# Kernel tuning notes

Hardware: AMD Instinct MI355X
Metric: run time of the kernel (lower is better)

## Reference

```python
import jax, jax.numpy as jnp
import numpy as np

MODES = (16, 16)

def setup_inputs() -> dict:
    key = jax.random.key(0)
    ks = jax.random.split(key, 8)
    B, Cin, Cout, H, W = 16, 64, 64, 128, 128
    scale = 1.0 / (Cin * Cout)
    return {
        "x": jax.random.normal(ks[0], (B, Cin, H, W), jnp.float32),
        "t_emb": jax.random.normal(ks[1], (B, 512), jnp.float32),
        "weight_real": jax.random.normal(ks[2], (Cin, Cout, *MODES), jnp.float32) * 2 * scale - scale,
        "weight_imag": jax.random.normal(ks[3], (Cin, Cout, *MODES), jnp.float32) * 2 * scale - scale,
        "bypass_w": jax.random.normal(ks[4], (Cout, Cin), jnp.float32) * 0.05,
        "bypass_b": jax.random.normal(ks[5], (Cout,), jnp.float32) * 0.05,
        "temb_w": jax.random.normal(ks[6], (Cin, 512), jnp.float32) * 0.02,
        "temb_b": jax.random.normal(ks[7], (Cin,), jnp.float32) * 0.02,
    }

def reference(x, t_emb, weight_real, weight_imag, bypass_w, bypass_b, temb_w, temb_b):
    mk, ml = MODES
    H, W = x.shape[-2:]
    xf = x.astype(jnp.float32)
    # truncated spectral conv: rfft2 (ortho), keep low-mode corner only
    x_fft = jnp.fft.rfftn(xf, axes=(-2, -1), norm="ortho")[:, :, :mk, :ml]
    weight = weight_real + 1j * weight_imag  # [i, o, k, l]
    out_fft = jnp.einsum("bikl,iokl->bokl", x_fft, weight)
    x_spec = jnp.fft.irfftn(out_fft, s=(H, W), axes=(-2, -1), norm="ortho")
    # 1x1 conv bypass
    byp = jnp.einsum("bihw,oi->bohw", xf, bypass_w) + bypass_b[None, :, None, None]
    out = jax.nn.gelu(x_spec + byp, approximate=False)
    # temb fusion: x + Linear(silu(temb))[:, :, None, None]
    silu_t = t_emb * jax.nn.sigmoid(t_emb)
    proj = silu_t @ temb_w.T + temb_b  # [B, C]
    out = out + proj[:, :, None, None]
    return out
```

## Files before the change

### kernel.cpp

```cpp
#include <hip/hip_runtime.h>
#include <cmath>

#define TWO_PI_128 0.04908738521234052f

typedef __attribute__((ext_vector_type(8))) short bf16x8;
typedef __attribute__((ext_vector_type(4))) float f32x4;

__device__ inline unsigned short f2bf(float v) {
  unsigned u = __float_as_uint(v);
  unsigned r = (u + 0x7FFFu + ((u >> 16) & 1u)) >> 16;
  return (unsigned short)r;
}

__global__ __launch_bounds__(256) void front_kernel(
    const float* __restrict__ x, float* __restrict__ xfr_t,
    float* __restrict__ xfi_t, const float* __restrict__ wr,
    const float* __restrict__ wi, float* __restrict__ wt_r,
    float* __restrict__ wt_i, const float* __restrict__ t_emb,
    const float* __restrict__ temb_w, const float* __restrict__ temb_b,
    float* __restrict__ proj, float2* __restrict__ Tck,
    unsigned short* __restrict__ Tspec) {
  __shared__ union SM {
    struct {
      unsigned short x1[32 * 136];
      float red[8 * 256];
    } f;
    float tile[32][33];
    struct {
      float silu[512];
      float part[64][4];
    } p;
  } sm;

  const int bid = blockIdx.x;
  const int t = threadIdx.x;

  if (bid >= 3088) {
    if (t < 128) {
      float dS, dC;
      sincosf(TWO_PI_128 * (float)t, &dS, &dC);
      float ck = 1.f, sk = 0.f;
      for (int k = 0; k < 16; ++k) {
        Tck[t * 16 + k] = make_float2(ck, sk);
        float tt = sk * dS, uu = ck * dS;
        ck = fmaf(ck, dC, -tt);
        sk = fmaf(sk, dC, uu);
      }
    } else {
      const int wn = t - 128;
      float st, ct;
      sincosf(TWO_PI_128 * (float)wn, &st, &ct);
#pragma unroll
      for (int half = 0; half < 2; ++half) {
        float ss, cc;
        sincosf(TWO_PI_128 * (float)(wn * (half * 8)), &ss, &cc);
        for (int j = 0; j < 8; ++j) {
          Tspec[wn * 32 + half * 8 + j] = f2bf(cc);
          Tspec[wn * 32 + 16 + half * 8 + j] = f2bf(-ss);
          float nc = cc * ct - ss * st;
          ss = ss * ct + cc * st;
          cc = nc;
        }
      }
    }
    return;
  }

  if (bid >= 3072) {
    const int b = bid - 3072;
    for (int j = t; j < 512; j += 256) {
      float v = t_emb[b * 512 + j];
      sm.p.silu[j] = v / (1.f + __expf(-v));
    }
    __syncthreads();
    const int o = t >> 2, part = t & 3;
    const float* wrow = temb_w + o * 512 + part * 128;
    const float* srow = sm.p.silu + part * 128;
    float acc = 0.f;
#pragma unroll 8
    for (int j = 0; j < 128; ++j) acc = fmaf(srow[j], wrow[j], acc);
    sm.p.part[o][part] = acc;
    __syncthreads();
    if (part == 0) {
      proj[b * 64 + o] = sm.p.part[o][0] + sm.p.part[o][1] + sm.p.part[o][2] +
                         sm.p.part[o][3] + temb_b[o];
    }
    return;
  }

  if (bid >= 1024) {
    const int flat = bid - 1024;
    const int tensor = flat >> 10;
    const int rem = flat & 1023;
    const int io0 = (rem >> 3) * 32, kl0 = (rem & 7) * 32;
    const float* src = tensor ? wi : wr;
    float* dst = tensor ? wt_i : wt_r;
    const int ty = t >> 3, tx = t & 7;
    float4 v = *(const float4*)(src + (size_t)(io0 + ty) * 256 + kl0 + 4 * tx);
    sm.tile[ty][4 * tx + 0] = v.x;
    sm.tile[ty][4 * tx + 1] = v.y;
    sm.tile[ty][4 * tx + 2] = v.z;
    sm.tile[ty][4 * tx + 3] = v.w;
    __syncthreads();
    float4 o;
    o.x = sm.tile[4 * tx + 0][ty];
    o.y = sm.tile[4 * tx + 1][ty];
    o.z = sm.tile[4 * tx + 2][ty];
    o.w = sm.tile[4 * tx + 3][ty];
    *(float4*)(dst + (size_t)(kl0 + ty) * 4096 + io0 + 4 * tx) = o;
    return;
  }

  const int plane = bid;
  const int wv = t >> 6, lane = t & 63, l15 = lane & 15, quad = lane >> 4;

  union U8 {
    bf16x8 v;
    unsigned short u[8];
  };

  float dC, dS;
  sincosf(TWO_PI_128 * (float)l15, &dS, &dC);

  U8 a_re[4], a_im[4];
#pragma unroll
  for (int ks = 0; ks < 4; ++ks) {
    const int w0 = ks * 32 + quad * 8;
    float c, s;
    sincosf(TWO_PI_128 * (float)((l15 * w0) & 127), &s, &c);
#pragma unroll
    for (int j = 0; j < 8; ++j) {
      a_re[ks].u[j] = f2bf(c);
      a_im[ks].u[j] = f2bf(-s);
      float nc = c * dC - s * dS;
      s = s * dC + c * dS;
      c = nc;
    }
  }

  const float* xp = x + (size_t)plane * 16384;
  f32x4 acc[2][2];
#pragma unroll
  for (int mt = 0; mt < 2; ++mt)
#pragma unroll
    for (int nt = 0; nt < 2; ++nt) acc[mt][nt] = (f32x4){0.f, 0.f, 0.f, 0.f};

#pragma unroll
  for (int ks = 0; ks < 4; ++ks) {
#pragma unroll
    for (int nt = 0; nt < 2; ++nt) {
      const float* src =
          xp + (size_t)((wv * 2 + nt) * 16 + l15) * 128 + ks * 32 + quad * 8;
      float4 v0 = *(const float4*)src;
      float4 v1 = *(const float4*)(src + 4);
      U8 bx;
      bx.u[0] = f2bf(v0.x);
      bx.u[1] = f2bf(v0.y);
      bx.u[2] = f2bf(v0.z);
      bx.u[3] = f2bf(v0.w);
      bx.u[4] = f2bf(v1.x);
      bx.u[5] = f2bf(v1.y);
      bx.u[6] = f2bf(v1.z);
      bx.u[7] = f2bf(v1.w);
      acc[0][nt] = __builtin_amdgcn_mfma_f32_16x16x32_bf16(a_re[ks].v, bx.v,
                                                           acc[0][nt], 0, 0, 0);
      acc[1][nt] = __builtin_amdgcn_mfma_f32_16x16x32_bf16(a_im[ks].v, bx.v,
                                                           acc[1][nt], 0, 0, 0);
    }
  }

#pragma unroll
  for (int mt = 0; mt < 2; ++mt)
#pragma unroll
    for (int nt = 0; nt < 2; ++nt)
#pragma unroll
      for (int r = 0; r < 4; ++r)
        sm.f.x1[(mt * 16 + quad * 4 + r) * 136 + (wv * 2 + nt) * 16 + l15] =
            f2bf(acc[mt][nt][r]);
  __syncthreads();

  f32x4 accre = (f32x4){0.f, 0.f, 0.f, 0.f};
  f32x4 accim = (f32x4){0.f, 0.f, 0.f, 0.f};
#pragma unroll
  for (int kl2 = 0; kl2 < 2; ++kl2) {
    const int ks2 = wv * 2 + kl2;
    const int hb = (ks2 & 3) * 32 + quad * 8;
    const int imh = ks2 >> 2;
    float c, s;
    sincosf(TWO_PI_128 * (float)((l15 * hb) & 127), &s, &c);
    U8 ar, ai;
#pragma unroll
    for (int j = 0; j < 8; ++j) {
      if (!imh) {
        ar.u[j] = f2bf(c);
        ai.u[j] = f2bf(-s);
      } else {
        ar.u[j] = f2bf(s);
        ai.u[j] = f2bf(c);
      }
      float nc = c * dC - s * dS;
      s = s * dC + c * dS;
      c = nc;
    }
    bf16x8 bfrag = *(const bf16x8*)(sm.f.x1 + (imh * 16 + l15) * 136 + hb);
    accre =
        __builtin_amdgcn_mfma_f32_16x16x32_bf16(ar.v, bfrag, accre, 0, 0, 0);
    accim =
        __builtin_amdgcn_mfma_f32_16x16x32_bf16(ai.v, bfrag, accim, 0, 0, 0);
  }
  *(f32x4*)(sm.f.red + (wv * 2) * 256 + lane * 4) = accre;
  *(f32x4*)(sm.f.red + (wv * 2 + 1) * 256 + lane * 4) = accim;
  __syncthreads();

  const float re =
      sm.f.red[t] + sm.f.red[512 + t] + sm.f.red[1024 + t] + sm.f.red[1536 + t];
  const float im = sm.f.red[256 + t] + sm.f.red[768 + t] + sm.f.red[1280 + t] +
                   sm.f.red[1792 + t];
  const int k = (t >> 6) * 4 + (t & 3), l = (t >> 2) & 15;
  xfr_t[(size_t)(k * 16 + l) * 1024 + plane] = re * 0.0078125f;
  xfi_t[(size_t)(k * 16 + l) * 1024 + plane] = im * 0.0078125f;
}

__global__ __launch_bounds__(1024) void modemix_kernel(
    const float* __restrict__ xfr_t, const float* __restrict__ xfi_t,
    const float* __restrict__ wt_r, const float* __restrict__ wt_i,
    float* __restrict__ ofr, float* __restrict__ ofi) {
  __shared__ float s_xr[1024], s_xi[1024];
  __shared__ float s_wr[4096], s_wi[4096];
  const int kl = blockIdx.x;
  const int t = threadIdx.x;
  if (t < 256)
    ((float4*)s_xr)[t] = ((const float4*)(xfr_t + (size_t)kl * 1024))[t];
  else if (t < 512)
    ((float4*)s_xi)[t - 256] =
        ((const float4*)(xfi_t + (size_t)kl * 1024))[t - 256];
  ((float4*)s_wr)[t] = ((const float4*)(wt_r + (size_t)kl * 4096))[t];
  ((float4*)s_wi)[t] = ((const float4*)(wt_i + (size_t)kl * 4096))[t];
  __syncthreads();
  const int b = t >> 6;
  const int o = t & 63;
  const float* xrp = s_xr + b * 64;
  const float* xip = s_xi + b * 64;
  float ar0 = 0.f, ar1 = 0.f, ai0 = 0.f, ai1 = 0.f;
#pragma unroll 4
  for (int i = 0; i < 64; ++i) {
    float wrv = s_wr[i * 64 + o], wiv = s_wi[i * 64 + o];
    float xr = xrp[i], xi = xip[i];
    ar0 = fmaf(xr, wrv, ar0);
    ar1 = fmaf(xi, wiv, ar1);
    ai0 = fmaf(xr, wiv, ai0);
    ai1 = fmaf(xi, wrv, ai1);
  }
  ofr[(size_t)(b * 64 + o) * 256 + kl] = ar0 - ar1;
  ofi[(size_t)(b * 64 + o) * 256 + kl] = ai0 + ai1;
}

__global__ __launch_bounds__(256, 4) void final_kernel(
    const float* __restrict__ x, const float* __restrict__ bw,
    const float* __restrict__ bb, const float* __restrict__ proj,
    const float* __restrict__ ofr, const float* __restrict__ ofi,
    const float2* __restrict__ Tck, const unsigned short* __restrict__ Tspec,
    float* __restrict__ out) {
#define AR 104
  __shared__ unsigned short s_A[64 * AR];
  __shared__ float s_bb[64];
  __shared__ float s_pb[64];
  const int h = blockIdx.x, b = blockIdx.y, t = threadIdx.x;
  const int wv = t >> 6, lane = t & 63;
  const int l15 = lane & 15, quad = lane >> 4;
  const int n0w = wv * 32;

  float xv[32];
  {
    const float* xbase = x + (size_t)b * 1048576 + (size_t)h * 128;
#pragma unroll
    for (int ks2 = 0; ks2 < 2; ++ks2)
#pragma unroll
      for (int nt = 0; nt < 2; ++nt)
#pragma unroll
        for (int j = 0; j < 8; ++j)
          xv[(ks2 * 2 + nt) * 8 + j] =
              xbase[(size_t)(ks2 * 32 + quad * 8 + j) * 16384 + n0w + nt * 16 +
                    l15];
  }

  bf16x8 tsf[2];
#pragma unroll
  for (int nt = 0; nt < 2; ++nt)
    tsf[nt] = *(const bf16x8*)(Tspec + (n0w + nt * 16 + l15) * 32 + quad * 8);

  if (t < 64)
    s_bb[t] = bb[t];
  else if (t < 128)
    s_pb[t - 64] = proj[b * 64 + (t - 64)];

  {
    const int o = t >> 2, q = t & 3;
    const float4* src = (const float4*)(bw + o * 64 + q * 16);
    unsigned int u[8];
#pragma unroll
    for (int m = 0; m < 4; ++m) {
      float4 v = src[m];
      u[2 * m] = (unsigned)f2bf(v.x) | ((unsigned)f2bf(v.y) << 16);
      u[2 * m + 1] = (unsigned)f2bf(v.z) | ((unsigned)f2bf(v.w) << 16);
    }
    uint4* dst = (uint4*)(s_A + o * AR + q * 16);
    dst[0] = make_uint4(u[0], u[1], u[2], u[3]);
    dst[1] = make_uint4(u[4], u[5], u[6], u[7]);
  }
  {
    const int o = t >> 2, lq = t & 3;
    const float* FR = ofr + (size_t)(b * 64 + o) * 256 + lq * 4;
    const float* FI = ofi + (size_t)(b * 64 + o) * 256 + lq * 4;
    const float2* tckrow = Tck + h * 16;
    float yr[4] = {0.f, 0.f, 0.f, 0.f};
    float yi[4] = {0.f, 0.f, 0.f, 0.f};
#pragma unroll 4
    for (int k = 0; k < 16; ++k) {
      float4 fr = *(const float4*)(FR + k * 16);
      float4 fi = *(const float4*)(FI + k * 16);
      const float2 cs = tckrow[k];
      const float ck = cs.x, sk = cs.y;
      yr[0] = fmaf(fr.x, ck, yr[0]);
      yr[0] = fmaf(-fi.x, sk, yr[0]);
      yi[0] = fmaf(fi.x, ck, yi[0]);
      yi[0] = fmaf(fr.x, sk, yi[0]);
      yr[1] = fmaf(fr.y, ck, yr[1]);
      yr[1] = fmaf(-fi.y, sk, yr[1]);
      yi[1] = fmaf(fi.y, ck, yi[1]);
      yi[1] = fmaf(fr.y, sk, yi[1]);
      yr[2] = fmaf(fr.z, ck, yr[2]);
      yr[2] = fmaf(-fi.z, sk, yr[2]);
      yi[2] = fmaf(fi.z, ck, yi[2]);
      yi[2] = fmaf(fr.z, sk, yi[2]);
      yr[3] = fmaf(fr.w, ck, yr[3]);
      yr[3] = fmaf(-fi.w, sk, yr[3]);
      yi[3] = fmaf(fi.w, ck, yi[3]);
      yi[3] = fmaf(fr.w, sk, yi[3]);
    }
    const float scl0 = (lq == 0) ? 0.0078125f : 0.015625f;
    unsigned ur0 = (unsigned)f2bf(yr[0] * scl0) |
                   ((unsigned)f2bf(yr[1] * 0.015625f) << 16);
    unsigned ur1 = (unsigned)f2bf(yr[2] * 0.015625f) |
                   ((unsigned)f2bf(yr[3] * 0.015625f) << 16);
    unsigned ui0 = (unsigned)f2bf(yi[0] * scl0) |
                   ((unsigned)f2bf(yi[1] * 0.015625f) << 16);
    unsigned ui1 = (unsigned)f2bf(yi[2] * 0.015625f) |
                   ((unsigned)f2bf(yi[3] * 0.015625f) << 16);
    *(uint2*)(s_A + o * AR + 64 + lq * 4) = make_uint2(ur0, ur1);
    *(uint2*)(s_A + o * AR + 64 + 16 + lq * 4) = make_uint2(ui0, ui1);
  }
  __syncthreads();

  f32x4 acc[4][2];
#pragma unroll
  for (int mt = 0; mt < 4; ++mt) {
    f32x4 bv = *(const f32x4*)(s_bb + mt * 16 + quad * 4);
    acc[mt][0] = bv;
    acc[mt][1] = bv;
  }

#pragma unroll
  for (int ks2 = 0; ks2 < 2; ++ks2) {
    union {
      bf16x8 v;
      unsigned short u[8];
    } bx[2];
#pragma unroll
    for (int nt = 0; nt < 2; ++nt)
#pragma unroll
      for (int j = 0; j < 8; ++j)
        bx[nt].u[j] = f2bf(xv[(ks2 * 2 + nt) * 8 + j]);
#pragma unroll
    for (int mt = 0; mt < 4; ++mt) {
      bf16x8 a =
          *(const bf16x8*)(s_A + (mt * 16 + l15) * AR + ks2 * 32 + quad * 8);
      acc[mt][0] = __builtin_amdgcn_mfma_f32_16x16x32_bf16(a, bx[0].v,
                                                           acc[mt][0], 0, 0, 0);
      acc[mt][1] = __builtin_amdgcn_mfma_f32_16x16x32_bf16(a, bx[1].v,
                                                           acc[mt][1], 0, 0, 0);
    }
  }

#pragma unroll
  for (int mt = 0; mt < 4; ++mt) {
    bf16x8 a = *(const bf16x8*)(s_A + (mt * 16 + l15) * AR + 64 + quad * 8);
    acc[mt][0] =
        __builtin_amdgcn_mfma_f32_16x16x32_bf16(a, tsf[0], acc[mt][0], 0, 0, 0);
    acc[mt][1] =
        __builtin_amdgcn_mfma_f32_16x16x32_bf16(a, tsf[1], acc[mt][1], 0, 0, 0);
  }

#pragma unroll
  for (int mt = 0; mt < 4; ++mt) {
    f32x4 pv = *(const f32x4*)(s_pb + mt * 16 + quad * 4);
#pragma unroll
    for (int nt = 0; nt < 2; ++nt) {
      const int wcol = n0w + nt * 16 + l15;
#pragma unroll
      for (int r = 0; r < 4; ++r) {
        const int o = mt * 16 + quad * 4 + r;
        float v = acc[mt][nt][r];
        float g = fmaf(0.5f * v, 1.f + erff(v * 0.70710678f), pv[r]);
        out[((size_t)(b * 64 + o) * 128 + h) * 128 + wcol] = g;
      }
    }
  }
#undef AR
}

extern "C" void kernel_launch(void* const* d_in, const int* in_sizes, int n_in,
                              void* d_out, int out_size, void* d_ws,
                              size_t ws_size, hipStream_t stream) {
  (void)in_sizes;
  (void)n_in;
  (void)out_size;
  (void)ws_size;
  const float* x = (const float*)d_in[0];
  const float* t_emb = (const float*)d_in[1];
  const float* wr = (const float*)d_in[2];
  const float* wi = (const float*)d_in[3];
  const float* bw = (const float*)d_in[4];
  const float* bb = (const float*)d_in[5];
  const float* tw = (const float*)d_in[6];
  const float* tb = (const float*)d_in[7];
  float* out = (float*)d_out;

  char* ws = (char*)d_ws;
  float* proj = (float*)(ws);
  float* ofr = (float*)(ws + ((size_t)1 << 20));
  float* ofi = (float*)(ws + ((size_t)2 << 20));
  float* xfr_t = (float*)(ws + ((size_t)3 << 20));
  float* xfi_t = (float*)(ws + ((size_t)4 << 20));
  float* wt_r = (float*)(ws + ((size_t)5 << 20));
  float* wt_i = (float*)(ws + ((size_t)9 << 20));
  float2* Tck = (float2*)(ws + ((size_t)13 << 20));
  unsigned short* Tspec = (unsigned short*)(ws + ((size_t)13 << 20) + 65536);

  front_kernel<<<3089, 256, 0, stream>>>(x, xfr_t, xfi_t, wr, wi, wt_r, wt_i,
                                         t_emb, tw, tb, proj, Tck, Tspec);
  modemix_kernel<<<256, 1024, 0, stream>>>(xfr_t, xfi_t, wt_r, wt_i, ofr, ofi);
  final_kernel<<<dim3(128, 16), 256, 0, stream>>>(x, bw, bb, proj, ofr, ofi,
                                                  Tck, Tspec, out);
}
```

Before: 168.4 us.

## Write bf16 copy of x in front kernel and read it in final kernel

The front kernel already converts x to bf16 for its DFT MFMA, and now also stores that bf16 copy in a transposed [b][h][c][w] layout in workspace. The final kernel reads the bf16 copy instead of re-reading fp32 x with strided loads and converting again, which halves the bytes it reads for x and drops the conversion. The cost is an extra 32 MB write in the front kernel. The final kernel also loses its min-blocks launch-bounds hint, so register allocation may change.

```diff
diff --git a/kernel.cpp b/kernel.cpp
--- a/kernel.cpp
+++ b/kernel.cpp
@@ -19,7 +19,7 @@
     float* __restrict__ wt_i, const float* __restrict__ t_emb,
     const float* __restrict__ temb_w, const float* __restrict__ temb_b,
     float* __restrict__ proj, float2* __restrict__ Tck,
-    unsigned short* __restrict__ Tspec) {
+    unsigned short* __restrict__ Tspec, unsigned short* __restrict__ xbf) {
   __shared__ union SM {
     struct {
       unsigned short x1[32 * 136];
@@ -112,6 +112,7 @@
   }
 
   const int plane = bid;
+  const int xb_ = plane >> 6, xi_ = plane & 63;
   const int wv = t >> 6, lane = t & 63, l15 = lane & 15, quad = lane >> 4;
 
   union U8 {
@@ -149,8 +150,8 @@
   for (int ks = 0; ks < 4; ++ks) {
 #pragma unroll
     for (int nt = 0; nt < 2; ++nt) {
-      const float* src =
-          xp + (size_t)((wv * 2 + nt) * 16 + l15) * 128 + ks * 32 + quad * 8;
+      const int row = (wv * 2 + nt) * 16 + l15;
+      const float* src = xp + (size_t)row * 128 + ks * 32 + quad * 8;
       float4 v0 = *(const float4*)src;
       float4 v1 = *(const float4*)(src + 4);
       U8 bx;
@@ -162,6 +163,8 @@
       bx.u[5] = f2bf(v1.y);
       bx.u[6] = f2bf(v1.z);
       bx.u[7] = f2bf(v1.w);
+      *(uint4*)(xbf + ((size_t)(xb_ * 128 + row) * 64 + xi_) * 128 + ks * 32 +
+                quad * 8) = *(const uint4*)&bx;
       acc[0][nt] = __builtin_amdgcn_mfma_f32_16x16x32_bf16(a_re[ks].v, bx.v,
                                                            acc[0][nt], 0, 0, 0);
       acc[1][nt] = __builtin_amdgcn_mfma_f32_16x16x32_bf16(a_im[ks].v, bx.v,
@@ -255,8 +258,8 @@
   ofi[(size_t)(b * 64 + o) * 256 + kl] = ai0 + ai1;
 }
 
-__global__ __launch_bounds__(256, 4) void final_kernel(
-    const float* __restrict__ x, const float* __restrict__ bw,
+__global__ __launch_bounds__(256) void final_kernel(
+    const unsigned short* __restrict__ xbf, const float* __restrict__ bw,
     const float* __restrict__ bb, const float* __restrict__ proj,
     const float* __restrict__ ofr, const float* __restrict__ ofi,
     const float2* __restrict__ Tck, const unsigned short* __restrict__ Tspec,
@@ -270,18 +273,22 @@
   const int l15 = lane & 15, quad = lane >> 4;
   const int n0w = wv * 32;
 
-  float xv[32];
+  union FB {
+    bf16x8 v;
+    unsigned short u[8];
+  };
+  FB bx[4];
   {
-    const float* xbase = x + (size_t)b * 1048576 + (size_t)h * 128;
+    const unsigned short* xb =
+        xbf + (size_t)(b * 128 + h) * 8192 + n0w + l15;
 #pragma unroll
     for (int ks2 = 0; ks2 < 2; ++ks2)
 #pragma unroll
-      for (int nt = 0; nt < 2; ++nt)
-#pragma unroll
-        for (int j = 0; j < 8; ++j)
-          xv[(ks2 * 2 + nt) * 8 + j] =
-              xbase[(size_t)(ks2 * 32 + quad * 8 + j) * 16384 + n0w + nt * 16 +
-                    l15];
+      for (int nt = 0; nt < 2; ++nt) {
+        const unsigned short* s = xb + (ks2 * 32 + quad * 8) * 128 + nt * 16;
+#pragma unroll
+        for (int j = 0; j < 8; ++j) bx[ks2 * 2 + nt].u[j] = s[j * 128];
+      }
   }
 
   bf16x8 tsf[2];
@@ -362,23 +369,14 @@
 
 #pragma unroll
   for (int ks2 = 0; ks2 < 2; ++ks2) {
-    union {
-      bf16x8 v;
-      unsigned short u[8];
-    } bx[2];
-#pragma unroll
-    for (int nt = 0; nt < 2; ++nt)
-#pragma unroll
-      for (int j = 0; j < 8; ++j)
-        bx[nt].u[j] = f2bf(xv[(ks2 * 2 + nt) * 8 + j]);
 #pragma unroll
     for (int mt = 0; mt < 4; ++mt) {
       bf16x8 a =
           *(const bf16x8*)(s_A + (mt * 16 + l15) * AR + ks2 * 32 + quad * 8);
-      acc[mt][0] = __builtin_amdgcn_mfma_f32_16x16x32_bf16(a, bx[0].v,
-                                                           acc[mt][0], 0, 0, 0);
-      acc[mt][1] = __builtin_amdgcn_mfma_f32_16x16x32_bf16(a, bx[1].v,
-                                                           acc[mt][1], 0, 0, 0);
+      acc[mt][0] = __builtin_amdgcn_mfma_f32_16x16x32_bf16(
+          a, bx[ks2 * 2 + 0].v, acc[mt][0], 0, 0, 0);
+      acc[mt][1] = __builtin_amdgcn_mfma_f32_16x16x32_bf16(
+          a, bx[ks2 * 2 + 1].v, acc[mt][1], 0, 0, 0);
     }
   }
 
@@ -436,10 +434,11 @@
   float* wt_i = (float*)(ws + ((size_t)9 << 20));
   float2* Tck = (float2*)(ws + ((size_t)13 << 20));
   unsigned short* Tspec = (unsigned short*)(ws + ((size_t)13 << 20) + 65536);
+  unsigned short* xbf = (unsigned short*)(ws + ((size_t)16 << 20));
 
   front_kernel<<<3089, 256, 0, stream>>>(x, xfr_t, xfi_t, wr, wi, wt_r, wt_i,
-                                         t_emb, tw, tb, proj, Tck, Tspec);
+                                         t_emb, tw, tb, proj, Tck, Tspec, xbf);
   modemix_kernel<<<256, 1024, 0, stream>>>(xfr_t, xfi_t, wt_r, wt_i, ofr, ofi);
-  final_kernel<<<dim3(128, 16), 256, 0, stream>>>(x, bw, bb, proj, ofr, ofi,
+  final_kernel<<<dim3(128, 16), 256, 0, stream>>>(xbf, bw, bb, proj, ofr, ofi,
                                                   Tck, Tspec, out);
 }
```

Result: slower. 173.8 us (+3.2%).

## Process two rows per final block and hoist front-kernel x loads

Applied to the files above, without the earlier changes.

The final kernel now handles two h rows per block, with half as many blocks. The bypass-weight conversion and the spectral inverse-FFT stage along k are shared across both rows, computing two Tck rows at once into a wider shared tile. The front kernel issues all of its x loads up front, before the twiddle sincos setup, so memory latency overlaps with that setup. The trade-off is fewer blocks and more registers per thread, with the min-occupancy launch bound dropped, so occupancy may fall.

```diff
diff --git a/kernel.cpp b/kernel.cpp
--- a/kernel.cpp
+++ b/kernel.cpp
@@ -119,6 +119,20 @@
     unsigned short u[8];
   };
 
+  float4 xv[16];
+  {
+    const float* xp = x + (size_t)plane * 16384;
+#pragma unroll
+    for (int ks = 0; ks < 4; ++ks)
+#pragma unroll
+      for (int nt = 0; nt < 2; ++nt) {
+        const float* src =
+            xp + (size_t)((wv * 2 + nt) * 16 + l15) * 128 + ks * 32 + quad * 8;
+        xv[(ks * 2 + nt) * 2 + 0] = *(const float4*)src;
+        xv[(ks * 2 + nt) * 2 + 1] = *(const float4*)(src + 4);
+      }
+  }
+
   float dC, dS;
   sincosf(TWO_PI_128 * (float)l15, &dS, &dC);
 
@@ -138,7 +152,6 @@
     }
   }
 
-  const float* xp = x + (size_t)plane * 16384;
   f32x4 acc[2][2];
 #pragma unroll
   for (int mt = 0; mt < 2; ++mt)
@@ -149,10 +162,8 @@
   for (int ks = 0; ks < 4; ++ks) {
 #pragma unroll
     for (int nt = 0; nt < 2; ++nt) {
-      const float* src =
-          xp + (size_t)((wv * 2 + nt) * 16 + l15) * 128 + ks * 32 + quad * 8;
-      float4 v0 = *(const float4*)src;
-      float4 v1 = *(const float4*)(src + 4);
+      const float4 v0 = xv[(ks * 2 + nt) * 2 + 0];
+      const float4 v1 = xv[(ks * 2 + nt) * 2 + 1];
       U8 bx;
       bx.u[0] = f2bf(v0.x);
       bx.u[1] = f2bf(v0.y);
@@ -255,34 +266,20 @@
   ofi[(size_t)(b * 64 + o) * 256 + kl] = ai0 + ai1;
 }
 
-__global__ __launch_bounds__(256, 4) void final_kernel(
+__global__ __launch_bounds__(256) void final_kernel(
     const float* __restrict__ x, const float* __restrict__ bw,
     const float* __restrict__ bb, const float* __restrict__ proj,
     const float* __restrict__ ofr, const float* __restrict__ ofi,
     const float2* __restrict__ Tck, const unsigned short* __restrict__ Tspec,
     float* __restrict__ out) {
-#define AR 104
+#define AR 136
   __shared__ unsigned short s_A[64 * AR];
   __shared__ float s_bb[64];
   __shared__ float s_pb[64];
-  const int h = blockIdx.x, b = blockIdx.y, t = threadIdx.x;
+  const int hp = blockIdx.x, b = blockIdx.y, t = threadIdx.x;
   const int wv = t >> 6, lane = t & 63;
   const int l15 = lane & 15, quad = lane >> 4;
   const int n0w = wv * 32;
-
-  float xv[32];
-  {
-    const float* xbase = x + (size_t)b * 1048576 + (size_t)h * 128;
-#pragma unroll
-    for (int ks2 = 0; ks2 < 2; ++ks2)
-#pragma unroll
-      for (int nt = 0; nt < 2; ++nt)
-#pragma unroll
-        for (int j = 0; j < 8; ++j)
-          xv[(ks2 * 2 + nt) * 8 + j] =
-              xbase[(size_t)(ks2 * 32 + quad * 8 + j) * 16384 + n0w + nt * 16 +
-                    l15];
-  }
 
   bf16x8 tsf[2];
 #pragma unroll
@@ -312,97 +309,115 @@
     const int o = t >> 2, lq = t & 3;
     const float* FR = ofr + (size_t)(b * 64 + o) * 256 + lq * 4;
     const float* FI = ofi + (size_t)(b * 64 + o) * 256 + lq * 4;
-    const float2* tckrow = Tck + h * 16;
-    float yr[4] = {0.f, 0.f, 0.f, 0.f};
-    float yi[4] = {0.f, 0.f, 0.f, 0.f};
+    const float2* tck0 = Tck + (hp * 2) * 16;
+    const float2* tck1 = Tck + (hp * 2 + 1) * 16;
+    float yr0[4] = {0.f, 0.f, 0.f, 0.f}, yi0[4] = {0.f, 0.f, 0.f, 0.f};
+    float yr1[4] = {0.f, 0.f, 0.f, 0.f}, yi1[4] = {0.f, 0.f, 0.f, 0.f};
 #pragma unroll 4
     for (int k = 0; k < 16; ++k) {
       float4 fr = *(const float4*)(FR + k * 16);
       float4 fi = *(const float4*)(FI + k * 16);
-      const float2 cs = tckrow[k];
-      const float ck = cs.x, sk = cs.y;
-      yr[0] = fmaf(fr.x, ck, yr[0]);
-      yr[0] = fmaf(-fi.x, sk, yr[0]);
-      yi[0] = fmaf(fi.x, ck, yi[0]);
-      yi[0] = fmaf(fr.x, sk, yi[0]);
-      yr[1] = fmaf(fr.y, ck, yr[1]);
-      yr[1] = fmaf(-fi.y, sk, yr[1]);
-      yi[1] = fmaf(fi.y, ck, yi[1]);
-      yi[1] = fmaf(fr.y, sk, yi[1]);
-      yr[2] = fmaf(fr.z, ck, yr[2]);
-      yr[2] = fmaf(-fi.z, sk, yr[2]);
-      yi[2] = fmaf(fi.z, ck, yi[2]);
-      yi[2] = fmaf(fr.z, sk, yi[2]);
-      yr[3] = fmaf(fr.w, ck, yr[3]);
-      yr[3] = fmaf(-fi.w, sk, yr[3]);
-      yi[3] = fmaf(fi.w, ck, yi[3]);
-      yi[3] = fmaf(fr.w, sk, yi[3]);
+      const float2 c0 = tck0[k], c1 = tck1[k];
+      const float frv[4] = {fr.x, fr.y, fr.z, fr.w};
+      const float fiv[4] = {fi.x, fi.y, fi.z, fi.w};
+#pragma unroll
+      for (int c = 0; c < 4; ++c) {
+        yr0[c] = fmaf(frv[c], c0.x, yr0[c]);
+        yr0[c] = fmaf(-fiv[c], c0.y, yr0[c]);
+        yi0[c] = fmaf(fiv[c], c0.x, yi0[c]);
+        yi0[c] = fmaf(frv[c], c0.y, yi0[c]);
+        yr1[c] = fmaf(frv[c], c1.x, yr1[c]);
+        yr1[c] = fmaf(-fiv[c], c1.y, yr1[c]);
+        yi1[c] = fmaf(fiv[c], c1.x, yi1[c]);
+        yi1[c] = fmaf(frv[c], c1.y, yi1[c]);
+      }
     }
     const float scl0 = (lq == 0) ? 0.0078125f : 0.015625f;
-    unsigned ur0 = (unsigned)f2bf(yr[0] * scl0) |
-                   ((unsigned)f2bf(yr[1] * 0.015625f) << 16);
-    unsigned ur1 = (unsigned)f2bf(yr[2] * 0.015625f) |
-                   ((unsigned)f2bf(yr[3] * 0.015625f) << 16);
-    unsigned ui0 = (unsigned)f2bf(yi[0] * scl0) |
-                   ((unsigned)f2bf(yi[1] * 0.015625f) << 16);
-    unsigned ui1 = (unsigned)f2bf(yi[2] * 0.015625f) |
-                   ((unsigned)f2bf(yi[3] * 0.015625f) << 16);
+    unsigned ur0 = (unsigned)f2bf(yr0[0] * scl0) |
+                   ((unsigned)f2bf(yr0[1] * 0.015625f) << 16);
+    unsigned ur1 = (unsigned)f2bf(yr0[2] * 0.015625f) |
+                   ((unsigned)f2bf(yr0[3] * 0.015625f) << 16);
+    unsigned ui0 = (unsigned)f2bf(yi0[0] * scl0) |
+                   ((unsigned)f2bf(yi0[1] * 0.015625f) << 16);
+    unsigned ui1 = (unsigned)f2bf(yi0[2] * 0.015625f) |
+                   ((unsigned)f2bf(yi0[3] * 0.015625f) << 16);
     *(uint2*)(s_A + o * AR + 64 + lq * 4) = make_uint2(ur0, ur1);
-    *(uint2*)(s_A + o * AR + 64 + 16 + lq * 4) = make_uint2(ui0, ui1);
+    *(uint2*)(s_A + o * AR + 80 + lq * 4) = make_uint2(ui0, ui1);
+    unsigned vr0 = (unsigned)f2bf(yr1[0] * scl0) |
+                   ((unsigned)f2bf(yr1[1] * 0.015625f) << 16);
+    unsigned vr1 = (unsigned)f2bf(yr1[2] * 0.015625f) |
+                   ((unsigned)f2bf(yr1[3] * 0.015625f) << 16);
+    unsigned vi0 = (unsigned)f2bf(yi1[0] * scl0) |
+                   ((unsigned)f2bf(yi1[1] * 0.015625f) << 16);
+    unsigned vi1 = (unsigned)f2bf(yi1[2] * 0.015625f) |
+                   ((unsigned)f2bf(yi1[3] * 0.015625f) << 16);
+    *(uint2*)(s_A + o * AR + 96 + lq * 4) = make_uint2(vr0, vr1);
+    *(uint2*)(s_A + o * AR + 112 + lq * 4) = make_uint2(vi0, vi1);
   }
   __syncthreads();
 
-  f32x4 acc[4][2];
-#pragma unroll
-  for (int mt = 0; mt < 4; ++mt) {
-    f32x4 bv = *(const f32x4*)(s_bb + mt * 16 + quad * 4);
-    acc[mt][0] = bv;
-    acc[mt][1] = bv;
-  }
-
-#pragma unroll
-  for (int ks2 = 0; ks2 < 2; ++ks2) {
-    union {
-      bf16x8 v;
-      unsigned short u[8];
-    } bx[2];
-#pragma unroll
-    for (int nt = 0; nt < 2; ++nt)
-#pragma unroll
-      for (int j = 0; j < 8; ++j)
-        bx[nt].u[j] = f2bf(xv[(ks2 * 2 + nt) * 8 + j]);
+#pragma unroll
+  for (int hh = 0; hh < 2; ++hh) {
+    const int h = hp * 2 + hh;
+
+    f32x4 acc[4][2];
 #pragma unroll
     for (int mt = 0; mt < 4; ++mt) {
-      bf16x8 a =
-          *(const bf16x8*)(s_A + (mt * 16 + l15) * AR + ks2 * 32 + quad * 8);
-      acc[mt][0] = __builtin_amdgcn_mfma_f32_16x16x32_bf16(a, bx[0].v,
+      f32x4 bv = *(const f32x4*)(s_bb + mt * 16 + quad * 4);
+      acc[mt][0] = bv;
+      acc[mt][1] = bv;
+    }
+
+    const float* xrow = x + (size_t)b * 1048576 + (size_t)h * 128 + n0w + l15;
+#pragma unroll
+    for (int ks = 0; ks < 64; ks += 32) {
+      union {
+        bf16x8 v;
+        unsigned short u[8];
+      } bx[2];
+#pragma unroll
+      for (int nt = 0; nt < 2; ++nt) {
+        float xv[8];
+#pragma unroll
+        for (int j = 0; j < 8; ++j)
+          xv[j] = xrow[(size_t)(ks + quad * 8 + j) * 16384 + nt * 16];
+#pragma unroll
+        for (int j = 0; j < 8; ++j) bx[nt].u[j] = f2bf(xv[j]);
+      }
+#pragma unroll
+      for (int mt = 0; mt < 4; ++mt) {
+        bf16x8 a =
+            *(const bf16x8*)(s_A + (mt * 16 + l15) * AR + ks + quad * 8);
+        acc[mt][0] = __builtin_amdgcn_mfma_f32_16x16x32_bf16(
+            a, bx[0].v, acc[mt][0], 0, 0, 0);
+        acc[mt][1] = __builtin_amdgcn_mfma_f32_16x16x32_bf16(
+            a, bx[1].v, acc[mt][1], 0, 0, 0);
+      }
+    }
+
+#pragma unroll
+    for (int mt = 0; mt < 4; ++mt) {
+      bf16x8 a = *(const bf16x8*)(s_A + (mt * 16 + l15) * AR + 64 + hh * 32 +
+                                  quad * 8);
+      acc[mt][0] = __builtin_amdgcn_mfma_f32_16x16x32_bf16(a, tsf[0],
                                                            acc[mt][0], 0, 0, 0);
-      acc[mt][1] = __builtin_amdgcn_mfma_f32_16x16x32_bf16(a, bx[1].v,
+      acc[mt][1] = __builtin_amdgcn_mfma_f32_16x16x32_bf16(a, tsf[1],
                                                            acc[mt][1], 0, 0, 0);
     }
-  }
-
-#pragma unroll
-  for (int mt = 0; mt < 4; ++mt) {
-    bf16x8 a = *(const bf16x8*)(s_A + (mt * 16 + l15) * AR + 64 + quad * 8);
-    acc[mt][0] =
-        __builtin_amdgcn_mfma_f32_16x16x32_bf16(a, tsf[0], acc[mt][0], 0, 0, 0);
-    acc[mt][1] =
-        __builtin_amdgcn_mfma_f32_16x16x32_bf16(a, tsf[1], acc[mt][1], 0, 0, 0);
-  }
-
-#pragma unroll
-  for (int mt = 0; mt < 4; ++mt) {
-    f32x4 pv = *(const f32x4*)(s_pb + mt * 16 + quad * 4);
-#pragma unroll
-    for (int nt = 0; nt < 2; ++nt) {
-      const int wcol = n0w + nt * 16 + l15;
-#pragma unroll
-      for (int r = 0; r < 4; ++r) {
-        const int o = mt * 16 + quad * 4 + r;
-        float v = acc[mt][nt][r];
-        float g = fmaf(0.5f * v, 1.f + erff(v * 0.70710678f), pv[r]);
-        out[((size_t)(b * 64 + o) * 128 + h) * 128 + wcol] = g;
+
+#pragma unroll
+    for (int mt = 0; mt < 4; ++mt) {
+      f32x4 pv = *(const f32x4*)(s_pb + mt * 16 + quad * 4);
+#pragma unroll
+      for (int nt = 0; nt < 2; ++nt) {
+        const int wcol = n0w + nt * 16 + l15;
+#pragma unroll
+        for (int r = 0; r < 4; ++r) {
+          const int o = mt * 16 + quad * 4 + r;
+          float v = acc[mt][nt][r];
+          float g = fmaf(0.5f * v, 1.f + erff(v * 0.70710678f), pv[r]);
+          out[((size_t)(b * 64 + o) * 128 + h) * 128 + wcol] = g;
+        }
       }
     }
   }
@@ -440,6 +455,6 @@
   front_kernel<<<3089, 256, 0, stream>>>(x, xfr_t, xfi_t, wr, wi, wt_r, wt_i,
                                          t_emb, tw, tb, proj, Tck, Tspec);
   modemix_kernel<<<256, 1024, 0, stream>>>(xfr_t, xfi_t, wt_r, wt_i, ofr, ofi);
-  final_kernel<<<dim3(128, 16), 256, 0, stream>>>(x, bw, bb, proj, ofr, ofi,
-                                                  Tck, Tspec, out);
+  final_kernel<<<dim3(64, 16), 256, 0, stream>>>(x, bw, bb, proj, ofr, ofi,
+                                                 Tck, Tspec, out);
 }
```

Measured after the change: 171.2 us. No clear change (+1.7%).

## Split final kernel over output-channel halves to double grid parallelism

Applied to the files above, without the earlier changes.

The final kernel now launches a third grid dimension of 2, so each block computes 32 of the 64 output channels. This shrinks per-block shared memory, accumulators and the inverse-DFT work per thread. The x tile is loaded inside the MFMA loop instead of being prefetched into 32 registers, and the occupancy hint in the launch bounds is dropped. The cost is that every x row is now read by two blocks, doubling x traffic for the bypass GEMM.

```diff
diff --git a/kernel.cpp b/kernel.cpp
--- a/kernel.cpp
+++ b/kernel.cpp
@@ -255,34 +255,21 @@
   ofi[(size_t)(b * 64 + o) * 256 + kl] = ai0 + ai1;
 }
 
-__global__ __launch_bounds__(256, 4) void final_kernel(
+__global__ __launch_bounds__(256) void final_kernel(
     const float* __restrict__ x, const float* __restrict__ bw,
     const float* __restrict__ bb, const float* __restrict__ proj,
     const float* __restrict__ ofr, const float* __restrict__ ofi,
     const float2* __restrict__ Tck, const unsigned short* __restrict__ Tspec,
     float* __restrict__ out) {
 #define AR 104
-  __shared__ unsigned short s_A[64 * AR];
+  __shared__ unsigned short s_A[32 * AR];
   __shared__ float s_bb[64];
   __shared__ float s_pb[64];
   const int h = blockIdx.x, b = blockIdx.y, t = threadIdx.x;
+  const int ob = blockIdx.z * 32;
   const int wv = t >> 6, lane = t & 63;
   const int l15 = lane & 15, quad = lane >> 4;
   const int n0w = wv * 32;
-
-  float xv[32];
-  {
-    const float* xbase = x + (size_t)b * 1048576 + (size_t)h * 128;
-#pragma unroll
-    for (int ks2 = 0; ks2 < 2; ++ks2)
-#pragma unroll
-      for (int nt = 0; nt < 2; ++nt)
-#pragma unroll
-        for (int j = 0; j < 8; ++j)
-          xv[(ks2 * 2 + nt) * 8 + j] =
-              xbase[(size_t)(ks2 * 32 + quad * 8 + j) * 16384 + n0w + nt * 16 +
-                    l15];
-  }
 
   bf16x8 tsf[2];
 #pragma unroll
@@ -294,9 +281,9 @@
   else if (t < 128)
     s_pb[t - 64] = proj[b * 64 + (t - 64)];
 
-  {
+  if (t < 128) {
     const int o = t >> 2, q = t & 3;
-    const float4* src = (const float4*)(bw + o * 64 + q * 16);
+    const float4* src = (const float4*)(bw + (ob + o) * 64 + q * 16);
     unsigned int u[8];
 #pragma unroll
     for (int m = 0; m < 4; ++m) {
@@ -309,72 +296,63 @@
     dst[1] = make_uint4(u[4], u[5], u[6], u[7]);
   }
   {
-    const int o = t >> 2, lq = t & 3;
-    const float* FR = ofr + (size_t)(b * 64 + o) * 256 + lq * 4;
-    const float* FI = ofi + (size_t)(b * 64 + o) * 256 + lq * 4;
+    const int o = t >> 3, lp = t & 7;
+    const float* FR = ofr + (size_t)(b * 64 + ob + o) * 256 + lp * 2;
+    const float* FI = ofi + (size_t)(b * 64 + ob + o) * 256 + lp * 2;
     const float2* tckrow = Tck + h * 16;
-    float yr[4] = {0.f, 0.f, 0.f, 0.f};
-    float yi[4] = {0.f, 0.f, 0.f, 0.f};
+    float yr0 = 0.f, yr1 = 0.f, yi0 = 0.f, yi1 = 0.f;
 #pragma unroll 4
     for (int k = 0; k < 16; ++k) {
-      float4 fr = *(const float4*)(FR + k * 16);
-      float4 fi = *(const float4*)(FI + k * 16);
+      float2 fr = *(const float2*)(FR + k * 16);
+      float2 fi = *(const float2*)(FI + k * 16);
       const float2 cs = tckrow[k];
       const float ck = cs.x, sk = cs.y;
-      yr[0] = fmaf(fr.x, ck, yr[0]);
-      yr[0] = fmaf(-fi.x, sk, yr[0]);
-      yi[0] = fmaf(fi.x, ck, yi[0]);
-      yi[0] = fmaf(fr.x, sk, yi[0]);
-      yr[1] = fmaf(fr.y, ck, yr[1]);
-      yr[1] = fmaf(-fi.y, sk, yr[1]);
-      yi[1] = fmaf(fi.y, ck, yi[1]);
-      yi[1] = fmaf(fr.y, sk, yi[1]);
-      yr[2] = fmaf(fr.z, ck, yr[2]);
-      yr[2] = fmaf(-fi.z, sk, yr[2]);
-      yi[2] = fmaf(fi.z, ck, yi[2]);
-      yi[2] = fmaf(fr.z, sk, yi[2]);
-      yr[3] = fmaf(fr.w, ck, yr[3]);
-      yr[3] = fmaf(-fi.w, sk, yr[3]);
-      yi[3] = fmaf(fi.w, ck, yi[3]);
-      yi[3] = fmaf(fr.w, sk, yi[3]);
-    }
-    const float scl0 = (lq == 0) ? 0.0078125f : 0.015625f;
-    unsigned ur0 = (unsigned)f2bf(yr[0] * scl0) |
-                   ((unsigned)f2bf(yr[1] * 0.015625f) << 16);
-    unsigned ur1 = (unsigned)f2bf(yr[2] * 0.015625f) |
-                   ((unsigned)f2bf(yr[3] * 0.015625f) << 16);
-    unsigned ui0 = (unsigned)f2bf(yi[0] * scl0) |
-                   ((unsigned)f2bf(yi[1] * 0.015625f) << 16);
-    unsigned ui1 = (unsigned)f2bf(yi[2] * 0.015625f) |
-                   ((unsigned)f2bf(yi[3] * 0.015625f) << 16);
-    *(uint2*)(s_A + o * AR + 64 + lq * 4) = make_uint2(ur0, ur1);
-    *(uint2*)(s_A + o * AR + 64 + 16 + lq * 4) = make_uint2(ui0, ui1);
+      yr0 = fmaf(fr.x, ck, yr0);
+      yr0 = fmaf(-fi.x, sk, yr0);
+      yi0 = fmaf(fi.x, ck, yi0);
+      yi0 = fmaf(fr.x, sk, yi0);
+      yr1 = fmaf(fr.y, ck, yr1);
+      yr1 = fmaf(-fi.y, sk, yr1);
+      yi1 = fmaf(fi.y, ck, yi1);
+      yi1 = fmaf(fr.y, sk, yi1);
+    }
+    const float sa = (lp == 0) ? 0.0078125f : 0.015625f;
+    unsigned ur = (unsigned)f2bf(yr0 * sa) |
+                  ((unsigned)f2bf(yr1 * 0.015625f) << 16);
+    unsigned ui = (unsigned)f2bf(yi0 * sa) |
+                  ((unsigned)f2bf(yi1 * 0.015625f) << 16);
+    *(unsigned*)(s_A + o * AR + 64 + lp * 2) = ur;
+    *(unsigned*)(s_A + o * AR + 80 + lp * 2) = ui;
   }
   __syncthreads();
 
-  f32x4 acc[4][2];
-#pragma unroll
-  for (int mt = 0; mt < 4; ++mt) {
-    f32x4 bv = *(const f32x4*)(s_bb + mt * 16 + quad * 4);
+  f32x4 acc[2][2];
+#pragma unroll
+  for (int mt = 0; mt < 2; ++mt) {
+    f32x4 bv = *(const f32x4*)(s_bb + ob + mt * 16 + quad * 4);
     acc[mt][0] = bv;
     acc[mt][1] = bv;
   }
 
-#pragma unroll
-  for (int ks2 = 0; ks2 < 2; ++ks2) {
+  const float* xrow = x + (size_t)b * 1048576 + (size_t)h * 128 + n0w + l15;
+#pragma unroll
+  for (int ks = 0; ks < 64; ks += 32) {
     union {
       bf16x8 v;
       unsigned short u[8];
     } bx[2];
 #pragma unroll
-    for (int nt = 0; nt < 2; ++nt)
+    for (int nt = 0; nt < 2; ++nt) {
+      float xv[8];
 #pragma unroll
       for (int j = 0; j < 8; ++j)
-        bx[nt].u[j] = f2bf(xv[(ks2 * 2 + nt) * 8 + j]);
-#pragma unroll
-    for (int mt = 0; mt < 4; ++mt) {
-      bf16x8 a =
-          *(const bf16x8*)(s_A + (mt * 16 + l15) * AR + ks2 * 32 + quad * 8);
+        xv[j] = xrow[(size_t)(ks + quad * 8 + j) * 16384 + nt * 16];
+#pragma unroll
+      for (int j = 0; j < 8; ++j) bx[nt].u[j] = f2bf(xv[j]);
+    }
+#pragma unroll
+    for (int mt = 0; mt < 2; ++mt) {
+      bf16x8 a = *(const bf16x8*)(s_A + (mt * 16 + l15) * AR + ks + quad * 8);
       acc[mt][0] = __builtin_amdgcn_mfma_f32_16x16x32_bf16(a, bx[0].v,
                                                            acc[mt][0], 0, 0, 0);
       acc[mt][1] = __builtin_amdgcn_mfma_f32_16x16x32_bf16(a, bx[1].v,
@@ -383,7 +361,7 @@
   }
 
 #pragma unroll
-  for (int mt = 0; mt < 4; ++mt) {
+  for (int mt = 0; mt < 2; ++mt) {
     bf16x8 a = *(const bf16x8*)(s_A + (mt * 16 + l15) * AR + 64 + quad * 8);
     acc[mt][0] =
         __builtin_amdgcn_mfma_f32_16x16x32_bf16(a, tsf[0], acc[mt][0], 0, 0, 0);
@@ -392,14 +370,14 @@
   }
 
 #pragma unroll
-  for (int mt = 0; mt < 4; ++mt) {
-    f32x4 pv = *(const f32x4*)(s_pb + mt * 16 + quad * 4);
+  for (int mt = 0; mt < 2; ++mt) {
+    f32x4 pv = *(const f32x4*)(s_pb + ob + mt * 16 + quad * 4);
 #pragma unroll
     for (int nt = 0; nt < 2; ++nt) {
       const int wcol = n0w + nt * 16 + l15;
 #pragma unroll
       for (int r = 0; r < 4; ++r) {
-        const int o = mt * 16 + quad * 4 + r;
+        const int o = ob + mt * 16 + quad * 4 + r;
         float v = acc[mt][nt][r];
         float g = fmaf(0.5f * v, 1.f + erff(v * 0.70710678f), pv[r]);
         out[((size_t)(b * 64 + o) * 128 + h) * 128 + wcol] = g;
@@ -440,6 +418,6 @@
   front_kernel<<<3089, 256, 0, stream>>>(x, xfr_t, xfi_t, wr, wi, wt_r, wt_i,
                                          t_emb, tw, tb, proj, Tck, Tspec);
   modemix_kernel<<<256, 1024, 0, stream>>>(xfr_t, xfi_t, wt_r, wt_i, ofr, ofi);
-  final_kernel<<<dim3(128, 16), 256, 0, stream>>>(x, bw, bb, proj, ofr, ofi,
-                                                  Tck, Tspec, out);
+  final_kernel<<<dim3(128, 16, 2), 256, 0, stream>>>(x, bw, bb, proj, ofr, ofi,
+                                                     Tck, Tspec, out);
 }
```

New measurement: 176.4 us. 4.8% more time.
